# Kernel tuning notes

Hardware: AMD Instinct MI355X
Metric: run time of the kernel (lower is better)

The kernel has to match this reference:

```python
import jax, jax.numpy as jnp
import numpy as np

B, S, E, D, DV = 4, 4096, 1024, 64, 1024
NEG_INF = jnp.inf


def setup_inputs() -> dict:
    key = jax.random.key(0)
    ks = jax.random.split(key, 5)
    x = jax.random.normal(ks[0], (B, S, E), dtype=jnp.float32)
    Wq = jax.random.normal(ks[1], (E, D), dtype=jnp.float32) * 0.02
    Wk = jax.random.normal(ks[2], (E, D), dtype=jnp.float32) * 0.02
    Wv = jax.random.normal(ks[3], (E, DV), dtype=jnp.float32) * 0.02
    bq = jnp.zeros((D,), dtype=jnp.float32)
    bk = jnp.zeros((D,), dtype=jnp.float32)
    bv = jnp.zeros((DV,), dtype=jnp.float32)
    pad = jax.random.uniform(ks[4], (B, S)) > 0.9
    mask_padding_x = jnp.where(pad, -jnp.inf, 0.0).astype(jnp.float32)
    return {"x": x, "Wq": Wq, "bq": bq, "Wk": Wk, "bk": bk,
            "Wv": Wv, "bv": bv, "mask_padding_x": mask_padding_x}


def _padding_mask(mask_padding_x):
    # Faithful replication of the torch mask-combination logic (self-attn: y mask == x mask).
    mask_x = mask_padding_x[:, :, None]   # [B, Sx, 1]
    mask_y = mask_padding_x[:, None, :]   # [B, 1, Sy]
    # (-inf)*(-inf)=+inf kept; 0*(-inf)=nan -> 0
    prod = jnp.nan_to_num(mask_x * mask_y, nan=0.0, posinf=jnp.inf)
    # one side padded -> -inf; both padded -> inf + (-inf) + (-inf) = nan -> 0; both valid -> 0
    final = jnp.nan_to_num(prod + mask_y + mask_x, nan=0.0, posinf=0.0, neginf=-jnp.inf)
    return final  # [B, Sx, Sy]


def _causal_mask(n):
    # create_mask: strictly-upper-triangular -inf, zeros on/below diagonal
    return jnp.triu(jnp.full((n, n), -jnp.inf, dtype=jnp.float32), k=1)


def reference(x, Wq, bq, Wk, bk, Wv, bv, mask_padding_x):
    # self-attention path (y = x), mask=True (causal), dropout in eval mode (identity)
    Q = jnp.einsum('bse,ed->bsd', x, Wq) + bq          # [B,S,D]
    K = jnp.einsum('bse,ed->bsd', x, Wk) + bk          # [B,S,D]
    V = jnp.einsum('bse,ev->bsv', x, Wv) + bv          # [B,S,DV]
    scale = 1.0 / jnp.sqrt(jnp.float32(D))
    QK = jnp.einsum('bqd,bkd->bqk', Q, K) * scale      # [B,S,S]
    QK = QK + _padding_mask(mask_padding_x)
    QK = QK + _causal_mask(x.shape[1])
    attn = jax.nn.softmax(QK, axis=-1)
    return jnp.einsum('bqk,bkv->bqv', attn, V)         # [B,S,DV]
```

## Files before the change

### kernel.cpp

```cpp
#include <hip/hip_runtime.h>
#include <stdint.h>

typedef __attribute__((ext_vector_type(8))) short short8;
typedef __attribute__((ext_vector_type(4))) float floatx4;

__device__ __forceinline__ unsigned short f2bf(float f) {
    unsigned u = __float_as_uint(f);
    u += 0x7FFFu + ((u >> 16) & 1u);
    return (unsigned short)(u >> 16);
}

__device__ __forceinline__ void gload_lds16(const void* g, void* l) {
    __builtin_amdgcn_global_load_lds(
        (const __attribute__((address_space(1))) unsigned int*)g,
        (__attribute__((address_space(3))) unsigned int*)l, 16, 0, 0);
}

__global__ __launch_bounds__(256)
void conv_x(const float* __restrict__ x, unsigned short* __restrict__ xb) {
    const size_t total = (size_t)16384 * 1024;
    for (size_t i = ((size_t)blockIdx.x * 256 + threadIdx.x) * 8; i < total;
         i += (size_t)2048 * 256 * 8) {
        float4 a = *(const float4*)&x[i];
        float4 b = *(const float4*)&x[i + 4];
        uint4 o;
        o.x = f2bf(a.x) | ((unsigned)f2bf(a.y) << 16);
        o.y = f2bf(a.z) | ((unsigned)f2bf(a.w) << 16);
        o.z = f2bf(b.x) | ((unsigned)f2bf(b.y) << 16);
        o.w = f2bf(b.z) | ((unsigned)f2bf(b.w) << 16);
        *(uint4*)&xb[i] = o;
    }
}

__global__ __launch_bounds__(256)
void transpose_all(const float* __restrict__ Wv, const float* __restrict__ Wq,
                   const float* __restrict__ Wk, unsigned short* __restrict__ Wt) {
    __shared__ float T[64][65];
    const int t = threadIdx.x;
    const int k0 = blockIdx.x * 64;
    const int y = blockIdx.y;
    const float* src; int N, n0, rowoff;
    if (y < 16)      { src = Wv; N = 1024; n0 = y * 64; rowoff = 0; }
    else if (y == 16){ src = Wq; N = 64;   n0 = 0;      rowoff = 1024; }
    else             { src = Wk; N = 64;   n0 = 0;      rowoff = 1088; }
    const int r = t >> 4, c4 = (t & 15) * 4;
#pragma unroll
    for (int i = 0; i < 4; i++) {
        float4 v = *(const float4*)&src[(size_t)(k0 + r + 16 * i) * N + n0 + c4];
        T[r + 16 * i][c4] = v.x; T[r + 16 * i][c4 + 1] = v.y;
        T[r + 16 * i][c4 + 2] = v.z; T[r + 16 * i][c4 + 3] = v.w;
    }
    __syncthreads();
#pragma unroll
    for (int i = 0; i < 4; i++) {
        const int n = rowoff + n0 + r + 16 * i;
        unsigned short b0 = f2bf(T[c4 + 0][r + 16 * i]);
        unsigned short b1 = f2bf(T[c4 + 1][r + 16 * i]);
        unsigned short b2 = f2bf(T[c4 + 2][r + 16 * i]);
        unsigned short b3 = f2bf(T[c4 + 3][r + 16 * i]);
        uint2 pv;
        pv.x = b0 | ((unsigned)b1 << 16);
        pv.y = b2 | ((unsigned)b3 << 16);
        *(uint2*)&Wt[(size_t)n * 1024 + k0 + c4] = pv;
    }
}

__global__ __launch_bounds__(576)
void pack_bias_all(const float* __restrict__ bv, const float* __restrict__ bq,
                   const float* __restrict__ bk, float* __restrict__ bf) {
    const int t = blockIdx.x * 576 + threadIdx.x;
    if (t < 1024) bf[t] = bv[t];
    else if (t < 1088) bf[t] = bq[t - 1024];
    else if (t < 1152) bf[t] = bk[t - 1088];
}

__global__ __launch_bounds__(256)
void gemm_fused(const unsigned short* __restrict__ A,
                const unsigned short* __restrict__ Bt,
                const float* __restrict__ bias,
                unsigned short* __restrict__ Vt,
                unsigned short* __restrict__ QKb)
{
    __shared__ unsigned short As[128 * 32];
    __shared__ unsigned short Bs[128 * 32];
    const int tid = threadIdx.x;
    const int w = tid >> 6, l = tid & 63;
    const int quad = l >> 4, l16 = l & 15;
    const int wr = w >> 1, wc = w & 1;
    const int m0 = blockIdx.x * 128, n0 = blockIdx.y * 128;

    const int lr = l >> 2, lk = (l & 3) * 8;
    const unsigned short* Ag0 = A + (size_t)(m0 + w * 16 + lr) * 1024 + lk;
    const unsigned short* Ag1 = Ag0 + (size_t)64 * 1024;
    const unsigned short* Bg0 = Bt + (size_t)(n0 + w * 16 + lr) * 1024 + lk;
    const unsigned short* Bg1 = Bg0 + (size_t)64 * 1024;
    unsigned short* Al0 = &As[w * 512 + l * 8];
    unsigned short* Bl0 = &Bs[w * 512 + l * 8];

    floatx4 acc[4][4];
#pragma unroll
    for (int i = 0; i < 4; i++)
#pragma unroll
        for (int j = 0; j < 4; j++) acc[i][j] = (floatx4)0.f;

    for (int e0 = 0; e0 < 1024; e0 += 32) {
        gload_lds16(Ag0 + e0, Al0);
        gload_lds16(Ag1 + e0, Al0 + 2048);
        gload_lds16(Bg0 + e0, Bl0);
        gload_lds16(Bg1 + e0, Bl0 + 2048);
        __syncthreads();
        short8 af[4], bf[4];
#pragma unroll
        for (int i = 0; i < 4; i++)
            af[i] = *(const short8*)&As[(wr * 64 + i * 16 + l16) * 32 + quad * 8];
#pragma unroll
        for (int j = 0; j < 4; j++)
            bf[j] = *(const short8*)&Bs[(wc * 64 + j * 16 + l16) * 32 + quad * 8];
#pragma unroll
        for (int i = 0; i < 4; i++)
#pragma unroll
            for (int j = 0; j < 4; j++)
                acc[i][j] = __builtin_amdgcn_mfma_f32_16x16x32_bf16(af[i], bf[j], acc[i][j], 0, 0, 0);
        __syncthreads();
    }

    const bool toQK = (n0 >= 1024);
#pragma unroll
    for (int j = 0; j < 4; j++) {
        const int n = n0 + wc * 64 + j * 16 + l16;
        const float bn = bias[n];
#pragma unroll
        for (int i = 0; i < 4; i++) {
            const int mb = m0 + wr * 64 + i * 16 + quad * 4;
            if (!toQK) {
                unsigned short t[4];
#pragma unroll
                for (int r = 0; r < 4; r++) t[r] = f2bf(acc[i][j][r] + bn);
                uint2 pv;
                pv.x = t[0] | ((unsigned)t[1] << 16);
                pv.y = t[2] | ((unsigned)t[3] << 16);
                *(uint2*)&Vt[(size_t)n * 16384 + mb] = pv;
            } else {
#pragma unroll
                for (int r = 0; r < 4; r++)
                    QKb[(size_t)(mb + r) * 128 + (n - 1024)] = f2bf(acc[i][j][r] + bn);
            }
        }
    }
}

__global__ __launch_bounds__(512, 4)
void attn_fused(const unsigned short* __restrict__ QKb,
                const unsigned short* __restrict__ Vt,
                const float* __restrict__ maskx,
                float* __restrict__ out)
{
    __shared__ unsigned short Qs[64 * 72];
    __shared__ unsigned short Ps[2][64 * 40];
    __shared__ float Ls[64];

    const int tid = threadIdx.x;
    const int wave = tid >> 6, lane = tid & 63;
    const int quad = lane >> 4, l16 = lane & 15;
    const int bid = blockIdx.x;
    const int dvh = bid & 1;
    const int b = (bid >> 1) & 3;
    const int t = bid >> 3;
    const int qt = (t < 32) ? (63 - t) : (t - 32);
    const int q0 = qt * 64;
    const int gq0 = b * 4096 + q0;

    if (tid < 64) Ls[tid] = 0.f;
    {
        const int r = tid >> 3, c = (tid & 7) * 8;
        uint4 v = *(const uint4*)&QKb[(size_t)(gq0 + r) * 128 + c];
        *(uint4*)&Qs[r * 72 + c] = v;
    }
    __syncthreads();

    const int rb = wave >> 1;
    const int kb = wave & 1;
    bool pq[4];
#pragma unroll
    for (int r = 0; r < 4; r++)
        pq[r] = maskx[b * 4096 + q0 + rb * 16 + quad * 4 + r] < -1e30f;

    const short8 qa0 = *(const short8*)&Qs[(rb * 16 + l16) * 72 + quad * 8];
    const short8 qa1 = *(const short8*)&Qs[(rb * 16 + l16) * 72 + 32 + quad * 8];

    floatx4 acc[4][4];
#pragma unroll
    for (int i = 0; i < 4; i++)
#pragma unroll
        for (int j = 0; j < 4; j++) acc[i][j] = (floatx4)0.f;
    float lacc[4] = {0.f, 0.f, 0.f, 0.f};

    const int niter = 2 * qt + 2;
    const float scale = 0.125f;
    const int dv0 = dvh * 512 + wave * 64;

    const unsigned short* kptr = QKb + ((size_t)(b * 4096 + kb * 16 + l16) * 128 + 64 + quad * 8);
    const float* mptr = maskx + b * 4096 + kb * 16 + l16;
    size_t voff[4];
#pragma unroll
    for (int cb = 0; cb < 4; cb++)
        voff[cb] = (size_t)(dv0 + cb * 16 + l16) * 16384 + b * 4096 + quad * 8;

    short8 kc0 = *(const short8*)kptr;
    short8 kc1 = *(const short8*)(kptr + 32);
    float mval = *mptr;

    for (int kt = 0; kt < niter; kt++) {
        const int k0 = kt * 32;
        short8 vb[4];
#pragma unroll
        for (int cb = 0; cb < 4; cb++)
            vb[cb] = *(const short8*)&Vt[voff[cb] + k0];
        floatx4 s = (floatx4)0.f;
        s = __builtin_amdgcn_mfma_f32_16x16x32_bf16(qa0, kc0, s, 0, 0, 0);
        s = __builtin_amdgcn_mfma_f32_16x16x32_bf16(qa1, kc1, s, 0, 0, 0);
        const bool pk = mval < -1e30f;
        {
            int kn = k0 + 32 + kb * 16 + l16;
            if (kn > 4095) kn = 4095;
            const unsigned short* np = QKb + ((size_t)(b * 4096 + kn) * 128 + 64 + quad * 8);
            kc0 = *(const short8*)np;
            kc1 = *(const short8*)(np + 32);
            mval = maskx[b * 4096 + kn];
        }
        const int kg = k0 + kb * 16 + l16;
        unsigned short pbits[4];
#pragma unroll
        for (int r = 0; r < 4; r++) {
            const int qrow = q0 + rb * 16 + quad * 4 + r;
            float p = 0.f;
            if (kg <= qrow && pk == pq[r]) p = __expf(s[r] * scale);
            lacc[r] += p;
            pbits[r] = f2bf(p);
        }
        unsigned short* Pw = Ps[kt & 1];
#pragma unroll
        for (int r = 0; r < 4; r++)
            Pw[(rb * 16 + quad * 4 + r) * 40 + kb * 16 + l16] = pbits[r];
        asm volatile("s_waitcnt lgkmcnt(0)" ::: "memory");
        __builtin_amdgcn_s_barrier();
        __builtin_amdgcn_sched_barrier(0);
        const unsigned short* Pr = Ps[kt & 1];
        short8 pa[4];
#pragma unroll
        for (int r2 = 0; r2 < 4; r2++)
            pa[r2] = *(const short8*)&Pr[(r2 * 16 + l16) * 40 + quad * 8];
#pragma unroll
        for (int cb = 0; cb < 4; cb++)
#pragma unroll
            for (int r2 = 0; r2 < 4; r2++)
                acc[r2][cb] = __builtin_amdgcn_mfma_f32_16x16x32_bf16(pa[r2], vb[cb], acc[r2][cb], 0, 0, 0);
    }

#pragma unroll
    for (int r = 0; r < 4; r++) {
        float v = lacc[r];
        v += __shfl_xor(v, 1);
        v += __shfl_xor(v, 2);
        v += __shfl_xor(v, 4);
        v += __shfl_xor(v, 8);
        if (l16 == 0) atomicAdd(&Ls[rb * 16 + quad * 4 + r], v);
    }
    __syncthreads();

#pragma unroll
    for (int r2 = 0; r2 < 4; r2++) {
#pragma unroll
        for (int r = 0; r < 4; r++) {
            const int qrow = q0 + r2 * 16 + quad * 4 + r;
            const float inv = 1.f / Ls[r2 * 16 + quad * 4 + r];
#pragma unroll
            for (int cb = 0; cb < 4; cb++)
                out[(size_t)(b * 4096 + qrow) * 1024 + dv0 + cb * 16 + l16] = acc[r2][cb][r] * inv;
        }
    }
}

extern "C" void kernel_launch(void* const* d_in, const int* in_sizes, int n_in,
                              void* d_out, int out_size, void* d_ws, size_t ws_size,
                              hipStream_t stream) {
    const float* x  = (const float*)d_in[0];
    const float* Wq = (const float*)d_in[1];
    const float* bq = (const float*)d_in[2];
    const float* Wk = (const float*)d_in[3];
    const float* bk = (const float*)d_in[4];
    const float* Wv = (const float*)d_in[5];
    const float* bv = (const float*)d_in[6];
    const float* mk = (const float*)d_in[7];
    float* out = (float*)d_out;

    char* ws = (char*)d_ws;
    unsigned short* Xb   = (unsigned short*)ws;
    unsigned short* Vt   = (unsigned short*)(ws + (33554432));
    unsigned short* Wt   = (unsigned short*)(ws + (67108864));
    unsigned short* QKb  = (unsigned short*)(ws + (69468160));
    float*          bfull= (float*)(ws + (73662464));

    conv_x<<<2048, 256, 0, stream>>>(x, Xb);
    transpose_all<<<dim3(16, 18), 256, 0, stream>>>(Wv, Wq, Wk, Wt);
    pack_bias_all<<<2, 576, 0, stream>>>(bv, bq, bk, bfull);

    gemm_fused<<<dim3(128, 9), 256, 0, stream>>>(Xb, Wt, bfull, Vt, QKb);

    attn_fused<<<dim3(4 * 64 * 2), 512, 0, stream>>>(QKb, Vt, mk, out);
}
```

Baseline: 391.4 us.

## Split long causal key ranges in two halves and combine partial results

```diff
diff --git a/kernel.cpp b/kernel.cpp
--- a/kernel.cpp
+++ b/kernel.cpp
@@ -153,7 +153,10 @@
 void attn_fused(const unsigned short* __restrict__ QKb,
                 const unsigned short* __restrict__ Vt,
                 const float* __restrict__ maskx,
-                float* __restrict__ out)
+                float* __restrict__ out,
+                float* __restrict__ A1,
+                float* __restrict__ L0,
+                float* __restrict__ L1)
 {
     __shared__ unsigned short Qs[64 * 72];
     __shared__ unsigned short Ps[2][64 * 40];
@@ -166,9 +169,13 @@
     const int dvh = bid & 1;
     const int b = (bid >> 1) & 3;
     const int t = bid >> 3;
-    const int qt = (t < 32) ? (63 - t) : (t - 32);
+    const int h = (t < 64) ? 0 : 1;
+    const int qt = (t < 32) ? (63 - t) : (t < 64) ? (t - 32) : (127 - t);
     const int q0 = qt * 64;
     const int gq0 = b * 4096 + q0;
+    const int klo = h ? 2048 : 0;
+    const int khi = h ? (q0 + 64) : ((q0 + 64 < 2048) ? (q0 + 64) : 2048);
+    const int niter = (khi - klo) >> 5;
 
     if (tid < 64) Ls[tid] = 0.f;
     {
@@ -195,12 +202,10 @@
         for (int j = 0; j < 4; j++) acc[i][j] = (floatx4)0.f;
     float lacc[4] = {0.f, 0.f, 0.f, 0.f};
 
-    const int niter = 2 * qt + 2;
     const float scale = 0.125f;
     const int dv0 = dvh * 512 + wave * 64;
 
-    const unsigned short* kptr = QKb + ((size_t)(b * 4096 + kb * 16 + l16) * 128 + 64 + quad * 8);
-    const float* mptr = maskx + b * 4096 + kb * 16 + l16;
+    const unsigned short* kptr = QKb + ((size_t)(b * 4096 + klo + kb * 16 + l16) * 128 + 64 + quad * 8);
     size_t voff[4];
 #pragma unroll
     for (int cb = 0; cb < 4; cb++)
@@ -208,10 +213,10 @@
 
     short8 kc0 = *(const short8*)kptr;
     short8 kc1 = *(const short8*)(kptr + 32);
-    float mval = *mptr;
+    float mval = maskx[b * 4096 + klo + kb * 16 + l16];
 
     for (int kt = 0; kt < niter; kt++) {
-        const int k0 = kt * 32;
+        const int k0 = klo + kt * 32;
         short8 vb[4];
 #pragma unroll
         for (int cb = 0; cb < 4; cb++)
@@ -268,15 +273,60 @@
     }
     __syncthreads();
 
-#pragma unroll
-    for (int r2 = 0; r2 < 4; r2++) {
-#pragma unroll
-        for (int r = 0; r < 4; r++) {
-            const int qrow = q0 + r2 * 16 + quad * 4 + r;
-            const float inv = 1.f / Ls[r2 * 16 + quad * 4 + r];
-#pragma unroll
-            for (int cb = 0; cb < 4; cb++)
-                out[(size_t)(b * 4096 + qrow) * 1024 + dv0 + cb * 16 + l16] = acc[r2][cb][r] * inv;
+    if (qt < 32) {
+#pragma unroll
+        for (int r2 = 0; r2 < 4; r2++) {
+#pragma unroll
+            for (int r = 0; r < 4; r++) {
+                const int qrow = q0 + r2 * 16 + quad * 4 + r;
+                const float inv = 1.f / Ls[r2 * 16 + quad * 4 + r];
+#pragma unroll
+                for (int cb = 0; cb < 4; cb++)
+                    out[(size_t)(b * 4096 + qrow) * 1024 + dv0 + cb * 16 + l16] = acc[r2][cb][r] * inv;
+            }
+        }
+    } else if (h == 0) {
+#pragma unroll
+        for (int r2 = 0; r2 < 4; r2++)
+#pragma unroll
+            for (int r = 0; r < 4; r++) {
+                const int qrow = q0 + r2 * 16 + quad * 4 + r;
+#pragma unroll
+                for (int cb = 0; cb < 4; cb++)
+                    out[(size_t)(b * 4096 + qrow) * 1024 + dv0 + cb * 16 + l16] = acc[r2][cb][r];
+            }
+        if (dvh == 0 && tid < 64) L0[b * 2048 + q0 - 2048 + tid] = Ls[tid];
+    } else {
+#pragma unroll
+        for (int r2 = 0; r2 < 4; r2++)
+#pragma unroll
+            for (int r = 0; r < 4; r++) {
+                const int pr = q0 - 2048 + r2 * 16 + quad * 4 + r;
+#pragma unroll
+                for (int cb = 0; cb < 4; cb++)
+                    A1[(size_t)(b * 2048 + pr) * 1024 + dv0 + cb * 16 + l16] = acc[r2][cb][r];
+            }
+        if (dvh == 0 && tid < 64) L1[b * 2048 + q0 - 2048 + tid] = Ls[tid];
+    }
+}
+
+__global__ __launch_bounds__(256)
+void combine(float* __restrict__ out, const float* __restrict__ A1,
+             const float* __restrict__ L0, const float* __restrict__ L1) {
+    const int wave = threadIdx.x >> 6, lane = threadIdx.x & 63;
+    for (int row = blockIdx.x * 4 + wave; row < 4 * 2048; row += gridDim.x * 4) {
+        const int b = row >> 11, qr = row & 2047;
+        const float inv = 1.f / (L0[row] + L1[row]);
+        float4* po = (float4*)&out[(size_t)(b * 4096 + 2048 + qr) * 1024];
+        const float4* pa = (const float4*)&A1[(size_t)row * 1024];
+        for (int c = lane; c < 256; c += 64) {
+            float4 o = po[c];
+            const float4 a = pa[c];
+            o.x = (o.x + a.x) * inv;
+            o.y = (o.y + a.y) * inv;
+            o.z = (o.z + a.z) * inv;
+            o.w = (o.w + a.w) * inv;
+            po[c] = o;
         }
     }
 }
@@ -300,6 +350,9 @@
     unsigned short* Wt   = (unsigned short*)(ws + (67108864));
     unsigned short* QKb  = (unsigned short*)(ws + (69468160));
     float*          bfull= (float*)(ws + (73662464));
+    float*          L0   = (float*)(ws + (73667072));
+    float*          L1   = (float*)(ws + (73699840));
+    float*          A1   = (float*)ws;
 
     conv_x<<<2048, 256, 0, stream>>>(x, Xb);
     transpose_all<<<dim3(16, 18), 256, 0, stream>>>(Wv, Wq, Wk, Wt);
@@ -307,5 +360,6 @@
 
     gemm_fused<<<dim3(128, 9), 256, 0, stream>>>(Xb, Wt, bfull, Vt, QKb);
 
-    attn_fused<<<dim3(4 * 64 * 2), 512, 0, stream>>>(QKb, Vt, mk, out);
-}
+    attn_fused<<<dim3(4 * 96 * 2), 512, 0, stream>>>(QKb, Vt, mk, out, A1, L0, L1);
+    combine<<<512, 256, 0, stream>>>(out, A1, L0, L1);
+}
```

New measurement: 447.5 us. 14.3% more time.
